# Optimization experiments

Hardware: AMD Instinct MI355X
Metric: run time of the kernel (lower is better)

Reference implementation:

```python
import jax, jax.numpy as jnp
import numpy as np
import math

D_MODEL = 1024
D_ATTN = 128
D_MID = 128
L = 4096

def setup_inputs() -> dict:
    key = jax.random.key(0)
    ks = jax.random.split(key, 5)
    scale = 1.0 / math.sqrt(D_MODEL)
    return {
        "x": jax.random.normal(ks[0], (L, D_MODEL), jnp.float32),
        "z": jax.random.normal(ks[1], (L, D_MODEL), jnp.float32),
        "Wq": jax.random.normal(ks[2], (D_MODEL, D_ATTN), jnp.float32) * scale,
        "bq": jnp.zeros((D_ATTN,), jnp.float32),
        "Wk": jax.random.normal(ks[3], (D_MODEL, D_ATTN), jnp.float32) * scale,
        "bk": jnp.zeros((D_ATTN,), jnp.float32),
        "Wv": jax.random.normal(ks[4], (D_MODEL, D_MID), jnp.float32) * scale,
        "bv": jnp.zeros((D_MID,), jnp.float32),
    }

def reference(x, z, Wq, bq, Wk, bk, Wv, bv):
    # q: [L_x, d_attn], k: [L_z, d_attn], v: [L_z, d_mid]
    q = x @ Wq + bq
    k = z @ Wk + bk
    v = z @ Wv + bv
    inv_sqrt_d = 1.0 / math.sqrt(D_ATTN)
    s = (q @ k.T) * inv_sqrt_d            # [L_x, L_z]
    y = jax.nn.softmax(s, axis=-1) @ v    # [L_x, d_mid]
    return y
```

## Files before the change

kernel.cpp:

```cpp
#include <hip/hip_runtime.h>
#include <hip/hip_bf16.h>

typedef __attribute__((ext_vector_type(8))) short short8;
typedef __attribute__((ext_vector_type(4))) float f32x4;
typedef __attribute__((ext_vector_type(8))) _Float16 half8;

#define L_SEQ 4096
#define DM    1024
#define DA    128
#define AZ    16

#define OFF_QB  786432
#define OFF_KF  1835008
#define OFF_VF  2883584
#define OFF_OA  4063232
#define OA_BYTES ((size_t)AZ * L_SEQ * DA * 2)

__device__ __forceinline__ short f2bf(float f) {
    union { float f; unsigned u; } v; v.f = f;
    unsigned u = v.u;
    u += 0x7FFFu + ((u >> 16) & 1u);
    return (short)(u >> 16);
}

__device__ __forceinline__ unsigned cvt_pk_bf16(float lo, float hi) {
    unsigned r;
    asm("v_cvt_pk_bf16_f32 %0, %1, %2" : "=v"(r) : "v"(lo), "v"(hi));
    return r;
}

typedef const __attribute__((address_space(1))) void g_void_t;
typedef __attribute__((address_space(3))) void l_void_t;
__device__ __forceinline__ void g2lds16(const void* g, void* l) {
    __builtin_amdgcn_global_load_lds((g_void_t*)g, (l_void_t*)l, 16, 0, 0);
}

__global__ __launch_bounds__(256) void prep_w_kernel(
    const float* __restrict__ Wq, const float* __restrict__ Wk,
    const float* __restrict__ Wv, short8* __restrict__ WTf)
{
    const int m = blockIdx.y, kidx = blockIdx.x;
    const float* __restrict__ W = (m == 0) ? Wq : (m == 1) ? Wk : Wv;
    __shared__ __align__(16) float Ws[32 * 132];
    const int t = threadIdx.x;
#pragma unroll
    for (int i = 0; i < 4; i++) {
        const int u = i * 256 + t;
        const int kk = u >> 5, n4 = (u & 31) * 4;
        *(f32x4*)&Ws[kk * 132 + n4] = *(const f32x4*)&W[(size_t)(kidx * 32 + kk) * DA + n4];
    }
    __syncthreads();
#pragma unroll
    for (int i = 0; i < 2; i++) {
        const int u = i * 256 + t;
        const int nt = u >> 6, lane = u & 63, l16 = lane & 15, quad = lane >> 4;
        short8 fr;
#pragma unroll
        for (int j = 0; j < 8; j++)
            fr[j] = f2bf(Ws[(quad * 8 + j) * 132 + nt * 16 + l16]);
        WTf[((size_t)(m * 32 + kidx) * 8 + nt) * 64 + lane] = fr;
    }
}

__global__ __launch_bounds__(256, 1) void qkv_kernel(
    const float* __restrict__ x, const float* __restrict__ z,
    const char* __restrict__ WTraw,
    const float* __restrict__ bq, const float* __restrict__ bk,
    const float* __restrict__ bv,
    short* __restrict__ qb, short8* __restrict__ kf, short8* __restrict__ vf)
{
    __shared__ __align__(16) char smem[2][32768];

    const int t = threadIdx.x;
    const int wave = t >> 6, lane = t & 63;
    const int l16 = lane & 15, quad = lane >> 4;
    const int mtile = wave >> 1, nhalf = wave & 1;
    const int isKV = blockIdx.y;
    const int m1 = isKV ? 1 : 0;
    const int row0 = blockIdx.x * 32;
    const int nbytes = isKV ? 32768 : 16384;

    const float* __restrict__ Am = isKV ? z : x;
    const float* ap = Am + (size_t)(row0 + mtile * 16 + l16) * DM + quad * 8;

    f32x4 acc1[4], acc2[4];
#pragma unroll
    for (int i = 0; i < 4; i++) {
        acc1[i] = (f32x4){0.f, 0.f, 0.f, 0.f};
        acc2[i] = (f32x4){0.f, 0.f, 0.f, 0.f};
    }

    auto stage = [&](int it2, int b) {
        const char* base1 = WTraw + (size_t)(m1 * 32 + it2 * 2) * 8192;
        const char* base2 = WTraw + (size_t)(2 * 32 + it2 * 2) * 8192;
#pragma unroll
        for (int i = 0; i < 8; i++) {
            const int off = i * 4096 + wave * 1024;
            if (off < nbytes) {
                const char* src = (off < 16384) ? (base1 + off) : (base2 + (off - 16384));
                g2lds16(src + lane * 16, &smem[b][off]);
            }
        }
    };

    f32x4 cur[4], nxt[4];
#pragma unroll
    for (int j = 0; j < 2; j++) {
        cur[j * 2]     = *(const f32x4*)(ap + j * 32);
        cur[j * 2 + 1] = *(const f32x4*)(ap + j * 32 + 4);
        nxt[j * 2]     = *(const f32x4*)(ap + 64 + j * 32);
        nxt[j * 2 + 1] = *(const f32x4*)(ap + 64 + j * 32 + 4);
    }

    stage(0, 0);
    __syncthreads();

#pragma unroll 1
    for (int it = 0; it < 16; it++) {
        const int b = it & 1;
        if (it + 1 < 16) stage(it + 1, b ^ 1);

        const int ipf = (it + 2 < 16) ? it + 2 : it;
        f32x4 fut[4];
#pragma unroll
        for (int j = 0; j < 2; j++) {
            fut[j * 2]     = *(const f32x4*)(ap + ipf * 64 + j * 32);
            fut[j * 2 + 1] = *(const f32x4*)(ap + ipf * 64 + j * 32 + 4);
        }

#pragma unroll
        for (int ss = 0; ss < 2; ss++) {
            short8 afr;
#pragma unroll
            for (int j = 0; j < 4; j++) {
                afr[j]     = f2bf(cur[ss * 2][j]);
                afr[4 + j] = f2bf(cur[ss * 2 + 1][j]);
            }
#pragma unroll
            for (int ntl = 0; ntl < 4; ntl++) {
                short8 bfr = *(const short8*)&smem[b][ss * 8192 + ((nhalf * 4 + ntl) * 64 + lane) * 16];
                acc1[ntl] = __builtin_amdgcn_mfma_f32_16x16x32_bf16(afr, bfr, acc1[ntl], 0, 0, 0);
            }
            if (isKV) {
#pragma unroll
                for (int ntl = 0; ntl < 4; ntl++) {
                    short8 bfr = *(const short8*)&smem[b][16384 + ss * 8192 + ((nhalf * 4 + ntl) * 64 + lane) * 16];
                    acc2[ntl] = __builtin_amdgcn_mfma_f32_16x16x32_bf16(afr, bfr, acc2[ntl], 0, 0, 0);
                }
            }
        }
        __syncthreads();
#pragma unroll
        for (int j = 0; j < 4; j++) { cur[j] = nxt[j]; nxt[j] = fut[j]; }
    }

    if (!isKV) {
        const float CL2E = 0.1275187669712930f;
#pragma unroll
        for (int ntl = 0; ntl < 4; ntl++) {
            const int col = nhalf * 64 + ntl * 16 + l16;
            const float bb = bq[col];
#pragma unroll
            for (int r = 0; r < 4; r++)
                qb[(size_t)(row0 + mtile * 16 + quad * 4 + r) * DA + col] =
                    f2bf((acc1[ntl][r] + bb) * CL2E);
        }
        return;
    }

    short* kT = (short*)&smem[0][0];
    short* vT = (short*)&smem[0][16384];
#pragma unroll
    for (int ntl = 0; ntl < 4; ntl++) {
        const int col = nhalf * 64 + ntl * 16 + l16;
        const float bbk = bk[col], bbv = bv[col];
#pragma unroll
        for (int r = 0; r < 4; r++) {
            const int rl = mtile * 16 + quad * 4 + r;
            kT[rl * 132 + col] = f2bf(acc1[ntl][r] + bbk);
            vT[rl * 132 + col] = f2bf(acc2[ntl][r] + bbv);
        }
    }
    __syncthreads();

    const int kg = blockIdx.x;
#pragma unroll
    for (int i = 0; i < 2; i++) {
        const int f = i * 256 + t;
        const int ks = f >> 7, nth = (f >> 6) & 1, ln = f & 63;
        const int lf = ln & 15, qf = ln >> 4;
        short8 fr;
#pragma unroll
        for (int j = 0; j < 8; j++)
            fr[j] = kT[(nth * 16 + lf) * 132 + ks * 32 + qf * 8 + j];
        kf[((size_t)(kg * 4 + ks) * 2 + nth) * 64 + ln] = fr;
    }
#pragma unroll
    for (int i = 0; i < 2; i++) {
        const int f = i * 256 + t;
        const int nt = f >> 6, ln = f & 63;
        const int lf = ln & 15, qf = ln >> 4;
        short8 fr;
#pragma unroll
        for (int j = 0; j < 8; j++)
            fr[j] = vT[(qf * 8 + j) * 132 + nt * 16 + lf];
        vf[((size_t)kg * 8 + nt) * 64 + ln] = fr;
    }
}

__global__ __launch_bounds__(256, 2) void attn_kernel(
    const short* __restrict__ qb, const char* __restrict__ kfg,
    const char* __restrict__ vfg, _Float16* __restrict__ OA,
    float* __restrict__ lA)
{
    __shared__ __align__(16) char kv[2][16384];

    const int t    = threadIdx.x;
    const int wave = t >> 6;
    const int lane = t & 63;
    const int l16  = lane & 15;
    const int quad = lane >> 4;
    const int qr0  = blockIdx.x * 128;
    const int g0   = blockIdx.y * 8;

    auto stage = [&](int g, int b) {
        const char* kb_ = kfg + (size_t)(g0 + g) * 8192;
        const char* vb_ = vfg + (size_t)(g0 + g) * 8192;
#pragma unroll
        for (int i = 0; i < 4; i++) {
            const int off = i * 4096 + wave * 1024;
            const char* src = (off < 8192) ? (kb_ + off) : (vb_ + (off - 8192));
            g2lds16(src + lane * 16, &kv[b][off]);
        }
    };

    stage(0, 0);

    short8 af[2][4];
#pragma unroll
    for (int mt = 0; mt < 2; mt++) {
        const short* qrow = qb + (size_t)(qr0 + wave * 32 + mt * 16 + l16) * DA + quad * 8;
#pragma unroll
        for (int ks = 0; ks < 4; ks++)
            af[mt][ks] = *(const short8*)(qrow + ks * 32);
    }

    short8 bones;
#pragma unroll
    for (int j = 0; j < 8; j++) bones[j] = (l16 == 0) ? (short)0x3F80 : (short)0;

    f32x4 O[2][9];
#pragma unroll
    for (int mt = 0; mt < 2; mt++)
#pragma unroll
        for (int i = 0; i < 9; i++) O[mt][i] = (f32x4){0.f, 0.f, 0.f, 0.f};

    __syncthreads();

#pragma unroll 1
    for (int g = 0; g < 8; g++) {
        const int b = g & 1;
        if (g + 1 < 8) stage(g + 1, b ^ 1);

        const char* kb_ = &kv[b][0];
        const char* vb_ = &kv[b][8192];

        f32x4 st[2][2];
#pragma unroll
        for (int zh = 0; zh < 2; zh++)
#pragma unroll
            for (int mt = 0; mt < 2; mt++) st[zh][mt] = (f32x4){0.f, 0.f, 0.f, 0.f};
#pragma unroll
        for (int ks = 0; ks < 4; ks++)
#pragma unroll
            for (int zh = 0; zh < 2; zh++) {
                const short8 kfr = *(const short8*)(kb_ + ((ks * 2 + zh) * 64 + lane) * 16);
                st[zh][0] = __builtin_amdgcn_mfma_f32_16x16x32_bf16(kfr, af[0][ks], st[zh][0], 0, 0, 0);
                st[zh][1] = __builtin_amdgcn_mfma_f32_16x16x32_bf16(kfr, af[1][ks], st[zh][1], 0, 0, 0);
            }

        short8 b2v[8];
#pragma unroll
        for (int nt = 0; nt < 8; nt++)
            b2v[nt] = *(const short8*)(vb_ + (nt * 64 + lane) * 16);

        short8 a2[2];
#pragma unroll
        for (int mt = 0; mt < 2; mt++) {
            unsigned x0 = cvt_pk_bf16(exp2f(st[0][mt][0]), exp2f(st[0][mt][1]));
            unsigned x1 = cvt_pk_bf16(exp2f(st[0][mt][2]), exp2f(st[0][mt][3]));
            unsigned y0 = cvt_pk_bf16(exp2f(st[1][mt][0]), exp2f(st[1][mt][1]));
            unsigned y1 = cvt_pk_bf16(exp2f(st[1][mt][2]), exp2f(st[1][mt][3]));
            asm volatile("v_permlane32_swap_b32 %0, %1" : "+v"(x0), "+v"(y0));
            asm volatile("v_permlane32_swap_b32 %0, %1" : "+v"(x1), "+v"(y1));
            const unsigned Asw0 = __builtin_amdgcn_ds_swizzle((int)x0, 0x401F);
            const unsigned Asw1 = __builtin_amdgcn_ds_swizzle((int)x1, 0x401F);
            const unsigned Bsw0 = __builtin_amdgcn_ds_swizzle((int)y0, 0x401F);
            const unsigned Bsw1 = __builtin_amdgcn_ds_swizzle((int)y1, 0x401F);
            const bool hiq = (quad & 1) != 0;
            union { short8 s; unsigned u[4]; } pa;
            pa.u[0] = hiq ? Bsw0 : x0;
            pa.u[1] = hiq ? Bsw1 : x1;
            pa.u[2] = hiq ? y0   : Asw0;
            pa.u[3] = hiq ? y1   : Asw1;
            a2[mt] = pa.s;
        }

#pragma unroll
        for (int nt = 0; nt < 8; nt++) {
            O[0][nt] = __builtin_amdgcn_mfma_f32_16x16x32_bf16(a2[0], b2v[nt], O[0][nt], 0, 0, 0);
            O[1][nt] = __builtin_amdgcn_mfma_f32_16x16x32_bf16(a2[1], b2v[nt], O[1][nt], 0, 0, 0);
        }
        O[0][8] = __builtin_amdgcn_mfma_f32_16x16x32_bf16(a2[0], bones, O[0][8], 0, 0, 0);
        O[1][8] = __builtin_amdgcn_mfma_f32_16x16x32_bf16(a2[1], bones, O[1][8], 0, 0, 0);
        __syncthreads();
    }

    const int rw = qr0 + wave * 32;
    _Float16* Ob = OA + (size_t)blockIdx.y * L_SEQ * DA;
#pragma unroll
    for (int mt = 0; mt < 2; mt++)
#pragma unroll
        for (int nt = 0; nt < 8; nt++)
#pragma unroll
            for (int r = 0; r < 4; r++)
                Ob[(size_t)(rw + mt * 16 + quad * 4 + r) * DA + nt * 16 + l16] =
                    (_Float16)O[mt][nt][r];
    if (l16 == 0) {
        float* lb = lA + (size_t)blockIdx.y * L_SEQ;
#pragma unroll
        for (int mt = 0; mt < 2; mt++)
#pragma unroll
            for (int r = 0; r < 4; r++)
                lb[rw + mt * 16 + quad * 4 + r] = O[mt][8][r];
    }
}

__global__ __launch_bounds__(256) void merge_kernel(
    const _Float16* __restrict__ OA, const float* __restrict__ lA,
    float* __restrict__ out)
{
    const int t = threadIdx.x;
    const int row = blockIdx.x * 16 + (t >> 4);
    const int cg = (t & 15) * 8;

    float acc[8];
#pragma unroll
    for (int j = 0; j < 8; j++) acc[j] = 0.f;
    float lsum = 0.f;
#pragma unroll
    for (int zz = 0; zz < AZ; zz++) {
        const half8 v = *(const half8*)&OA[((size_t)zz * L_SEQ + row) * DA + cg];
#pragma unroll
        for (int j = 0; j < 8; j++) acc[j] += (float)v[j];
        lsum += lA[(size_t)zz * L_SEQ + row];
    }
    const float inv = 1.f / lsum;
    f32x4 o0, o1;
#pragma unroll
    for (int j = 0; j < 4; j++) { o0[j] = acc[j] * inv; o1[j] = acc[4 + j] * inv; }
    f32x4* dst = (f32x4*)&out[(size_t)row * DA + cg];
    dst[0] = o0;
    dst[1] = o1;
}

extern "C" void kernel_launch(void* const* d_in, const int* in_sizes, int n_in,
                              void* d_out, int out_size, void* d_ws, size_t ws_size,
                              hipStream_t stream) {
    (void)in_sizes; (void)n_in; (void)out_size; (void)ws_size;
    const float* x  = (const float*)d_in[0];
    const float* z  = (const float*)d_in[1];
    const float* Wq = (const float*)d_in[2];
    const float* bq = (const float*)d_in[3];
    const float* Wk = (const float*)d_in[4];
    const float* bk = (const float*)d_in[5];
    const float* Wv = (const float*)d_in[6];
    const float* bv = (const float*)d_in[7];
    float* out = (float*)d_out;

    short8*   WTf = (short8*)d_ws;
    short*    qb  = (short*)((char*)d_ws + OFF_QB);
    short8*   kf  = (short8*)((char*)d_ws + OFF_KF);
    short8*   vf  = (short8*)((char*)d_ws + OFF_VF);
    _Float16* OA  = (_Float16*)((char*)d_ws + OFF_OA);
    float*    lA  = (float*)((char*)d_ws + OFF_OA + OA_BYTES);

    prep_w_kernel<<<dim3(32, 3), 256, 0, stream>>>(Wq, Wk, Wv, WTf);
    qkv_kernel<<<dim3(128, 2), 256, 0, stream>>>(x, z, (const char*)WTf,
                                                 bq, bk, bv, qb, kf, vf);
    attn_kernel<<<dim3(32, AZ), 256, 0, stream>>>(qb, (const char*)kf,
                                                  (const char*)vf, OA, lA);
    merge_kernel<<<256, 256, 0, stream>>>(OA, lA, out);
}
```

Before: 126.7 us.

## Load V fragments directly from global and use permlane16 swaps for P relayout

The attention loop now stages only K tiles into LDS (halving the LDS buffer) and reads V fragments straight from global memory into registers at the start of each iteration, so the V loads can overlap with the QK^T MFMAs. The P-matrix relayout replaces four ds_swizzle operations plus lane-conditional selects with two v_permlane16_swap instructions. This cuts LDS footprint and traffic and removes cross-lane LDS-path shuffles, but it exposes global-load latency for V inside the loop and relies on the V data being cache-resident across the blocks that share it.

```diff
diff --git a/kernel.cpp b/kernel.cpp
--- a/kernel.cpp
+++ b/kernel.cpp
@@ -213,7 +213,7 @@
     const char* __restrict__ vfg, _Float16* __restrict__ OA,
     float* __restrict__ lA)
 {
-    __shared__ __align__(16) char kv[2][16384];
+    __shared__ __align__(16) char kv[2][8192];
 
     const int t    = threadIdx.x;
     const int wave = t >> 6;
@@ -224,14 +224,9 @@
     const int g0   = blockIdx.y * 8;
 
     auto stage = [&](int g, int b) {
-        const char* kb_ = kfg + (size_t)(g0 + g) * 8192;
-        const char* vb_ = vfg + (size_t)(g0 + g) * 8192;
-#pragma unroll
-        for (int i = 0; i < 4; i++) {
-            const int off = i * 4096 + wave * 1024;
-            const char* src = (off < 8192) ? (kb_ + off) : (vb_ + (off - 8192));
-            g2lds16(src + lane * 16, &kv[b][off]);
-        }
+        const char* kb_ = kfg + (size_t)(g0 + g) * 8192 + wave * 2048;
+        g2lds16(kb_ + lane * 16,        &kv[b][wave * 2048]);
+        g2lds16(kb_ + 1024 + lane * 16, &kv[b][wave * 2048 + 1024]);
     };
 
     stage(0, 0);
@@ -262,8 +257,13 @@
         const int b = g & 1;
         if (g + 1 < 8) stage(g + 1, b ^ 1);
 
+        const short8* vgp = (const short8*)(vfg + (size_t)(g0 + g) * 8192);
+        short8 b2v[8];
+#pragma unroll
+        for (int nt = 0; nt < 8; nt++)
+            b2v[nt] = vgp[nt * 64 + lane];
+
         const char* kb_ = &kv[b][0];
-        const char* vb_ = &kv[b][8192];
 
         f32x4 st[2][2];
 #pragma unroll
@@ -278,11 +278,6 @@
                 st[zh][0] = __builtin_amdgcn_mfma_f32_16x16x32_bf16(kfr, af[0][ks], st[zh][0], 0, 0, 0);
                 st[zh][1] = __builtin_amdgcn_mfma_f32_16x16x32_bf16(kfr, af[1][ks], st[zh][1], 0, 0, 0);
             }
-
-        short8 b2v[8];
-#pragma unroll
-        for (int nt = 0; nt < 8; nt++)
-            b2v[nt] = *(const short8*)(vb_ + (nt * 64 + lane) * 16);
 
         short8 a2[2];
 #pragma unroll
@@ -293,16 +288,13 @@
             unsigned y1 = cvt_pk_bf16(exp2f(st[1][mt][2]), exp2f(st[1][mt][3]));
             asm volatile("v_permlane32_swap_b32 %0, %1" : "+v"(x0), "+v"(y0));
             asm volatile("v_permlane32_swap_b32 %0, %1" : "+v"(x1), "+v"(y1));
-            const unsigned Asw0 = __builtin_amdgcn_ds_swizzle((int)x0, 0x401F);
-            const unsigned Asw1 = __builtin_amdgcn_ds_swizzle((int)x1, 0x401F);
-            const unsigned Bsw0 = __builtin_amdgcn_ds_swizzle((int)y0, 0x401F);
-            const unsigned Bsw1 = __builtin_amdgcn_ds_swizzle((int)y1, 0x401F);
-            const bool hiq = (quad & 1) != 0;
+            asm volatile("v_permlane16_swap_b32 %0, %1" : "+v"(x0), "+v"(y0));
+            asm volatile("v_permlane16_swap_b32 %0, %1" : "+v"(x1), "+v"(y1));
             union { short8 s; unsigned u[4]; } pa;
-            pa.u[0] = hiq ? Bsw0 : x0;
-            pa.u[1] = hiq ? Bsw1 : x1;
-            pa.u[2] = hiq ? y0   : Asw0;
-            pa.u[3] = hiq ? y1   : Asw1;
+            pa.u[0] = x0;
+            pa.u[1] = x1;
+            pa.u[2] = y0;
+            pa.u[3] = y1;
             a2[mt] = pa.s;
         }
 
```

New measurement: 126.3 us. No clear change (-0.3%).
